# Kernel tuning notes

Hardware: AMD Instinct MI355X
Metric: run time of the kernel (lower is better)

## Reference

```python
import jax, jax.numpy as jnp
import numpy as np

N_NODES = 50000
N_EDGES = 500000
D_IN = 128
D_HID = 128
C = 1.0          # curvature (same for every layer)
MIN_NORM = 1e-15
MAX_TANH_ARG = 15.0
PROJ_EPS = 4e-3  # float32 boundary eps used by hgcn PoincareBall.proj


def _artanh(x):
    x = jnp.clip(x, -1.0 + 1e-7, 1.0 - 1e-7)
    return 0.5 * (jnp.log1p(x) - jnp.log1p(-x))


def _tanh(x):
    return jnp.tanh(jnp.clip(x, -MAX_TANH_ARG, MAX_TANH_ARG))


def _norm(x):
    return jnp.maximum(jnp.linalg.norm(x, axis=-1, keepdims=True), MIN_NORM)


def proj(x, c):
    # clip points to stay strictly inside the Poincare ball
    n = _norm(x)
    maxnorm = (1.0 - PROJ_EPS) / jnp.sqrt(c)
    return jnp.where(n > maxnorm, x / n * maxnorm, x)


def expmap0(u, c):
    sc = jnp.sqrt(c)
    n = _norm(u)
    return _tanh(sc * n) * u / (sc * n)


def logmap0(p, c):
    sc = jnp.sqrt(c)
    n = _norm(p)
    return _artanh(sc * n) * p / (sc * n)


def mobius_add(x, y, c):
    x2 = jnp.sum(x * x, -1, keepdims=True)
    y2 = jnp.sum(y * y, -1, keepdims=True)
    xy = jnp.sum(x * y, -1, keepdims=True)
    num = (1.0 + 2.0 * c * xy + c * y2) * x + (1.0 - c * x2) * y
    den = 1.0 + 2.0 * c * xy + c * c * x2 * y2
    return num / jnp.maximum(den, MIN_NORM)


def mobius_matvec(m, x, c):
    sc = jnp.sqrt(c)
    xn = _norm(x)
    mx = x @ m.T                                   # [N, out]
    mxn = _norm(mx)
    res = _tanh(mxn / xn * _artanh(sc * xn)) * mx / (mxn * sc)
    is_zero = jnp.all(mx == 0.0, axis=-1, keepdims=True)
    return jnp.where(is_zero, jnp.zeros_like(res), res)


def hyp_linear(x, W, b, c):
    h = proj(mobius_matvec(W, x, c), c)
    hyp_bias = proj(expmap0(b[None, :], c), c)     # proj_tan0 is identity on the ball
    return proj(mobius_add(h, hyp_bias, c), c)


def hyp_agg(x, src, dst, edge_weight, c):
    x_tan = logmap0(x, c)                          # [N, d] tangent at origin
    msg = edge_weight[:, None] * x_tan[src]        # [E, d] gather + scale
    agg = jax.ops.segment_sum(msg, dst, num_segments=N_NODES)  # spmm(adj, x_tan)
    return proj(expmap0(agg, c), c)


def hyp_act(x, c_in, c_out):
    xt = jax.nn.relu(logmap0(x, c_in))
    return proj(expmap0(xt, c_out), c_out)


def setup_inputs() -> dict:
    key = jax.random.key(0)
    ks = jax.random.split(key, 8)
    x = jax.random.normal(ks[0], (N_NODES, D_IN), dtype=jnp.float32) * 0.1
    src = jax.random.randint(ks[1], (N_EDGES,), 0, N_NODES)
    dst = jax.random.randint(ks[2], (N_EDGES,), 0, N_NODES)
    edge_weight = jax.random.uniform(ks[3], (N_EDGES,), dtype=jnp.float32) * 0.1
    s1 = 1.0 / np.sqrt(D_IN)
    W1 = jax.random.normal(ks[4], (D_HID, D_IN), dtype=jnp.float32) * s1
    b1 = jax.random.normal(ks[5], (D_HID,), dtype=jnp.float32) * 0.01
    W2 = jax.random.normal(ks[6], (D_HID, D_HID), dtype=jnp.float32) * s1
    b2 = jax.random.normal(ks[7], (D_HID,), dtype=jnp.float32) * 0.01
    return {"x": x, "src": src, "dst": dst, "edge_weight": edge_weight,
            "W1": W1, "b1": b1, "W2": W2, "b2": b2}


def reference(x, src, dst, edge_weight, W1, b1, W2, b2):
    c = jnp.float32(C)
    # HGCN.encode: proj_tan0 (identity for PoincareBall) -> expmap0 -> proj
    h = proj(expmap0(x, c), c)
    # layer 1: HypLinear -> HypAgg -> HypAct
    h = hyp_linear(h, W1, b1, c)
    h = hyp_agg(h, src, dst, edge_weight, c)
    h = hyp_act(h, c, c)
    # layer 2
    h = hyp_linear(h, W2, b2, c)
    h = hyp_agg(h, src, dst, edge_weight, c)
    h = hyp_act(h, c, c)
    return h
```

## Files before the change

kernel.cpp:

```cpp
#include <hip/hip_runtime.h>
#include <math.h>

#define MIN_NORM 1e-15f
#define MAXNORM  0.996f
#define ARTANH_CLIP 0.99999988f

typedef __bf16 bf16x8 __attribute__((ext_vector_type(8)));
typedef float  f32x4  __attribute__((ext_vector_type(4)));

union FragU { ushort u[8]; uint4 q; bf16x8 v; };

__device__ __forceinline__ float wave_sum(float v) {
#pragma unroll
    for (int off = 32; off > 0; off >>= 1) v += __shfl_xor(v, off, 64);
    return v;
}

__device__ __forceinline__ float artanh_c(float x) {
    x = fminf(fmaxf(x, -ARTANH_CLIP), ARTANH_CLIP);
    return 0.5f * (log1pf(x) - log1pf(-x));
}

__device__ __forceinline__ float tanh_c(float x) {
    return tanhf(fminf(fmaxf(x, -15.f), 15.f));
}

__device__ __forceinline__ float proj_factor(float n2) {
    float n = fmaxf(sqrtf(n2), MIN_NORM);
    return (n > MAXNORM) ? (MAXNORM / n) : 1.f;
}

__device__ __forceinline__ unsigned short f2bf(float f) {
    unsigned u = __float_as_uint(f);
    return (unsigned short)((u + 0x7fffu + ((u >> 16) & 1u)) >> 16);
}
__device__ __forceinline__ float bf2f(unsigned short h) {
    return __uint_as_float((unsigned)h << 16);
}

__device__ __forceinline__ void red16_f4(float4& v) {
#pragma unroll
    for (int off = 1; off < 16; off <<= 1) {
        v.x += __shfl_xor(v.x, off, 64);
        v.y += __shfl_xor(v.y, off, 64);
        v.z += __shfl_xor(v.z, off, 64);
        v.w += __shfl_xor(v.w, off, 64);
    }
}

__device__ __forceinline__ float bcast_row(const float4& v, int r) {
    const int src = (r >> 2) << 4;
    const float a = __shfl(v.x, src, 64);
    const float b = __shfl(v.y, src, 64);
    const float c = __shfl(v.z, src, 64);
    const float d = __shfl(v.w, src, 64);
    const float lo = (r & 1) ? b : a;
    const float hi = (r & 1) ? d : c;
    return (r & 2) ? hi : lo;
}

__device__ __forceinline__ void pack_w4(const float4 w4, int o, int k, char* out) {
    ushort4 h, l;
    h.x = f2bf(w4.x); l.x = f2bf(w4.x - bf2f(h.x));
    h.y = f2bf(w4.y); l.y = f2bf(w4.y - bf2f(h.y));
    h.z = f2bf(w4.z); l.z = f2bf(w4.z - bf2f(h.z));
    h.w = f2bf(w4.w); l.w = f2bf(w4.w - bf2f(h.w));
    const int prow = ((o & 7) << 4) | (o >> 3);
    const unsigned byte = (unsigned)((prow << 8) + (k << 1)) ^ (unsigned)((prow & 7) << 4);
    *reinterpret_cast<ushort4*>(out + byte) = h;
    *reinterpret_cast<ushort4*>(out + 32768 + byte) = l;
}

__global__ __launch_bounds__(256)
void setup_kernel(const float* __restrict__ W1, const float* __restrict__ W2,
                  char* __restrict__ g1, char* __restrict__ g2,
                  const float* __restrict__ b1, const float* __restrict__ b2,
                  float* __restrict__ hb1, float* __restrict__ hb2,
                  const int* __restrict__ dst, int* __restrict__ cnt, int E) {
    const int b = blockIdx.x;
    if (b < 32) {
        const float* W = (b < 16) ? W1 : W2;
        char* out = (b < 16) ? g1 : g2;
        const int i = (((b & 15) * 256) + threadIdx.x) * 4;
        pack_w4(*reinterpret_cast<const float4*>(&W[i]), i >> 7, i & 127, out);
    } else if (b == 32) {
        if (threadIdx.x < 64) {
            const int lane = threadIdx.x;
#pragma unroll
            for (int j = 0; j < 2; ++j) {
                const float* bb = j ? b2 : b1;
                float* hb = j ? hb2 : hb1;
                float v0 = bb[lane], v1 = bb[lane + 64];
                float n2 = wave_sum(v0 * v0 + v1 * v1);
                float n = fmaxf(sqrtf(n2), MIN_NORM);
                float sc = tanh_c(n) / n;
                sc *= proj_factor(sc * sc * n2);
                hb[lane] = v0 * sc;
                hb[lane + 64] = v1 * sc;
            }
        }
    } else {
        const int e = (b - 33) * 256 + threadIdx.x;
        if (e < E) atomicAdd(&cnt[dst[e]], 1);
    }
}


__global__ void scan1(const int* __restrict__ cnt, int* __restrict__ ptr,
                      int* __restrict__ bsum, int N) {
    __shared__ int s[256];
    const int t = threadIdx.x;
    const int i = blockIdx.x * 256 + t;
    int v = (i < N) ? cnt[i] : 0;
    s[t] = v;
    __syncthreads();
#pragma unroll
    for (int off = 1; off < 256; off <<= 1) {
        int add = (t >= off) ? s[t - off] : 0;
        __syncthreads();
        s[t] += add;
        __syncthreads();
    }
    if (i < N) ptr[i] = s[t] - v;
    if (t == 255) bsum[blockIdx.x] = s[255];
}

__global__ void scan2(const int* __restrict__ bsum, int* __restrict__ bscan, int nb) {
    __shared__ int s[256];
    const int t = threadIdx.x;
    int v = (t < nb) ? bsum[t] : 0;
    s[t] = v;
    __syncthreads();
#pragma unroll
    for (int off = 1; off < 256; off <<= 1) {
        int add = (t >= off) ? s[t - off] : 0;
        __syncthreads();
        s[t] += add;
        __syncthreads();
    }
    bscan[t] = s[t] - v;
}

__global__ void scan3(const int* __restrict__ bscan, int* __restrict__ ptr,
                      int* __restrict__ cursor, int N, int E) {
    const int i = blockIdx.x * blockDim.x + threadIdx.x;
    if (i < N) {
        const int p = ptr[i] + bscan[i >> 8];
        ptr[i] = p;
        cursor[i] = p;
    }
    if (i == 0) ptr[N] = E;
}

__global__ void scatter_kernel(const int* __restrict__ src, const int* __restrict__ dst,
                               const float* __restrict__ ew, int* __restrict__ cursor,
                               unsigned* __restrict__ epk, int E) {
    int e = blockIdx.x * blockDim.x + threadIdx.x;
    if (e >= E) return;
    int pos = atomicAdd(&cursor[dst[e]], 1);
    epk[pos] = ((unsigned)src[e] << 16) | (unsigned)f2bf(ew[e]);
}

template <bool PRELUDE, bool BF16OUT>
__global__ __launch_bounds__(1024, 4)
void hyp_linear_tan_mfma(const float* __restrict__ xin, const char* __restrict__ gWpack,
                         const float* __restrict__ hb, void* __restrict__ xtan,
                         int n_rows) {
    __shared__ __align__(16) char sW[65536];

    const int tid = threadIdx.x;
    const int lane = tid & 63, wid = tid >> 6;
    const int r15 = lane & 15, g = lane >> 4;

    const int tiles = (n_rows + 15) >> 4;
    const int tile = blockIdx.x + gridDim.x * wid;
    const bool active = (tile < tiles);
    const int rowbase = tile << 4;
    const int myrow = rowbase + r15;
    const bool rok = active && (myrow < n_rows);
    const float* xr = xin + (size_t)myrow * 128 + g * 8;

    float4 xa[4], xb[4];
#pragma unroll
    for (int kc = 0; kc < 4; ++kc) {
        if (rok) {
            xa[kc] = *reinterpret_cast<const float4*>(xr + kc * 32);
            xb[kc] = *reinterpret_cast<const float4*>(xr + kc * 32 + 4);
        } else {
            xa[kc] = make_float4(0.f, 0.f, 0.f, 0.f);
            xb[kc] = xa[kc];
        }
    }

    {
        const uint4* gsrc = reinterpret_cast<const uint4*>(gWpack);
        uint4* ldst = reinterpret_cast<uint4*>(sW);
#pragma unroll
        for (int i = 0; i < 4; ++i) ldst[tid + i * 1024] = gsrc[tid + i * 1024];
    }

    float yb[8];
    {
        const float4 yba = *reinterpret_cast<const float4*>(&hb[r15 * 8]);
        const float4 ybb = *reinterpret_cast<const float4*>(&hb[r15 * 8 + 4]);
        yb[0] = yba.x; yb[1] = yba.y; yb[2] = yba.z; yb[3] = yba.w;
        yb[4] = ybb.x; yb[5] = ybb.y; yb[6] = ybb.z; yb[7] = ybb.w;
    }
    float y2p = 0.f;
#pragma unroll
    for (int t = 0; t < 8; ++t) y2p += yb[t] * yb[t];
#pragma unroll
    for (int off = 1; off < 16; off <<= 1) y2p += __shfl_xor(y2p, off, 64);
    const float y2 = y2p;

    __syncthreads();
    if (!active) return;

    bf16x8 ah[4], al[4];
    float ss = 0.f;
#pragma unroll
    for (int kc = 0; kc < 4; ++kc) {
        const float4 a = xa[kc], b = xb[kc];
        ss += a.x * a.x + a.y * a.y + a.z * a.z + a.w * a.w
            + b.x * b.x + b.y * b.y + b.z * b.z + b.w * b.w;
        ah[kc][0] = (__bf16)a.x; al[kc][0] = (__bf16)(a.x - (float)ah[kc][0]);
        ah[kc][1] = (__bf16)a.y; al[kc][1] = (__bf16)(a.y - (float)ah[kc][1]);
        ah[kc][2] = (__bf16)a.z; al[kc][2] = (__bf16)(a.z - (float)ah[kc][2]);
        ah[kc][3] = (__bf16)a.w; al[kc][3] = (__bf16)(a.w - (float)ah[kc][3]);
        ah[kc][4] = (__bf16)b.x; al[kc][4] = (__bf16)(b.x - (float)ah[kc][4]);
        ah[kc][5] = (__bf16)b.y; al[kc][5] = (__bf16)(b.y - (float)ah[kc][5]);
        ah[kc][6] = (__bf16)b.z; al[kc][6] = (__bf16)(b.z - (float)ah[kc][6]);
        ah[kc][7] = (__bf16)b.w; al[kc][7] = (__bf16)(b.w - (float)ah[kc][7]);
    }
    ss += __shfl_xor(ss, 16, 64);
    ss += __shfl_xor(ss, 32, 64);

    f32x4 acc[8];
#pragma unroll
    for (int ct = 0; ct < 8; ++ct) acc[ct] = (f32x4){0.f, 0.f, 0.f, 0.f};

    const unsigned lswz = (unsigned)((r15 & 7) << 4);
#pragma unroll
    for (int kc = 0; kc < 4; ++kc) {
#pragma unroll
        for (int ct = 0; ct < 8; ++ct) {
            const unsigned byte =
                ((unsigned)((ct << 12) + (r15 << 8) + (kc << 6) + (g << 4))) ^ lswz;
            FragU bh, bl;
            bh.q = *reinterpret_cast<const uint4*>(sW + byte);
            bl.q = *reinterpret_cast<const uint4*>(sW + 32768 + byte);
            acc[ct] = __builtin_amdgcn_mfma_f32_16x16x32_bf16(ah[kc], bh.v, acc[ct], 0, 0, 0);
            acc[ct] = __builtin_amdgcn_mfma_f32_16x16x32_bf16(ah[kc], bl.v, acc[ct], 0, 0, 0);
            acc[ct] = __builtin_amdgcn_mfma_f32_16x16x32_bf16(al[kc], bh.v, acc[ct], 0, 0, 0);
        }
    }

    float4 r2 = make_float4(0.f, 0.f, 0.f, 0.f);
    float4 xyv = make_float4(0.f, 0.f, 0.f, 0.f);
#pragma unroll
    for (int ct = 0; ct < 8; ++ct) {
        r2.x += acc[ct][0] * acc[ct][0];
        r2.y += acc[ct][1] * acc[ct][1];
        r2.z += acc[ct][2] * acc[ct][2];
        r2.w += acc[ct][3] * acc[ct][3];
        xyv.x += acc[ct][0] * yb[ct];
        xyv.y += acc[ct][1] * yb[ct];
        xyv.z += acc[ct][2] * yb[ct];
        xyv.w += acc[ct][3] * yb[ct];
    }
    red16_f4(r2);
    red16_f4(xyv);

    const float rn2 = bcast_row(r2, r15);
    const float xyr = bcast_row(xyv, r15);
    const float n2v = ss;

    const float n = fmaxf(sqrtf(n2v), MIN_NORM);
    float sc = 1.f;
    if (PRELUDE) {
        sc = tanh_c(n) / n;
        sc *= proj_factor(sc * sc * n2v);
    }
    const float xn = fmaxf(sc * n, MIN_NORM);
    const float mxn = fmaxf(sc * sqrtf(rn2), MIN_NORM);
    const float s = tanh_c(mxn / xn * artanh_c(xn));
    const float sl0 = (s * sc) / mxn;
    float m2 = rn2 * sl0 * sl0;
    const float f = proj_factor(m2);
    const float scl = sl0 * f;
    m2 *= f * f;
    const float xy = scl * xyr;
    const float cx = 1.f + 2.f * xy + y2;
    const float cy = 1.f - m2;
    const float rdn = 1.f / fmaxf(1.f + 2.f * xy + m2 * y2, MIN_NORM);
    const float A = cx * scl * rdn;
    const float B = cy * rdn;
    const float on2 = A * A * rn2 + 2.f * A * B * xyr + B * B * y2;
    const float f2 = proj_factor(on2);
    const float onn = fmaxf(sqrtf(on2) * f2, MIN_NORM);
    const float slg = artanh_c(onn) / onn;
    const float P = slg * f2 * A;
    const float Q = slg * f2 * B;

#pragma unroll
    for (int reg = 0; reg < 4; ++reg) {
        const float Pr = __shfl(P, 4 * g + reg, 64);
        const float Qr = __shfl(Q, 4 * g + reg, 64);
        const int row = rowbase + 4 * g + reg;
        if (row < n_rows) {
            float v[8];
#pragma unroll
            for (int ct = 0; ct < 8; ++ct)
                v[ct] = fmaf(Pr, acc[ct][reg], Qr * yb[ct]);
            if (BF16OUT) {
                uint4 pk;
                pk.x = (unsigned)f2bf(v[0]) | ((unsigned)f2bf(v[1]) << 16);
                pk.y = (unsigned)f2bf(v[2]) | ((unsigned)f2bf(v[3]) << 16);
                pk.z = (unsigned)f2bf(v[4]) | ((unsigned)f2bf(v[5]) << 16);
                pk.w = (unsigned)f2bf(v[6]) | ((unsigned)f2bf(v[7]) << 16);
                *reinterpret_cast<uint4*>((char*)xtan + (size_t)row * 256 + r15 * 16) = pk;
            } else {
                float* orow = (float*)xtan + (size_t)row * 128 + r15 * 8;
                *reinterpret_cast<float4*>(orow) = make_float4(v[0], v[1], v[2], v[3]);
                *reinterpret_cast<float4*>(orow + 4) = make_float4(v[4], v[5], v[6], v[7]);
            }
        }
    }
}

__global__ __launch_bounds__(256)
void gather_act(const char* __restrict__ xt, const int* __restrict__ ptr,
                const unsigned* __restrict__ epk, float* __restrict__ out, int n_rows) {
    const int v = blockIdx.x * 4 + (threadIdx.x >> 6);
    if (v >= n_rows) return;
    const int lane = threadIdx.x & 63, l2 = lane << 1;
    const unsigned loff = (unsigned)lane << 2;
    const int beg = ptr[v], end = ptr[v + 1];
    float a0 = 0.f, a1 = 0.f, c0 = 0.f, c1 = 0.f;
    int i = beg;
    for (; i + 3 < end; i += 4) {
        const unsigned p0 = epk[i], p1 = epk[i + 1], p2 = epk[i + 2], p3 = epk[i + 3];
        const unsigned u0 = *reinterpret_cast<const unsigned*>(xt + ((p0 >> 16) << 8) + loff);
        const unsigned u1 = *reinterpret_cast<const unsigned*>(xt + ((p1 >> 16) << 8) + loff);
        const unsigned u2 = *reinterpret_cast<const unsigned*>(xt + ((p2 >> 16) << 8) + loff);
        const unsigned u3 = *reinterpret_cast<const unsigned*>(xt + ((p3 >> 16) << 8) + loff);
        const float w0 = __uint_as_float(p0 << 16), w1 = __uint_as_float(p1 << 16);
        const float w2 = __uint_as_float(p2 << 16), w3 = __uint_as_float(p3 << 16);
        a0 = fmaf(w0, __uint_as_float(u0 << 16), a0);
        a1 = fmaf(w0, __uint_as_float(u0 & 0xffff0000u), a1);
        c0 = fmaf(w1, __uint_as_float(u1 << 16), c0);
        c1 = fmaf(w1, __uint_as_float(u1 & 0xffff0000u), c1);
        a0 = fmaf(w2, __uint_as_float(u2 << 16), a0);
        a1 = fmaf(w2, __uint_as_float(u2 & 0xffff0000u), a1);
        c0 = fmaf(w3, __uint_as_float(u3 << 16), c0);
        c1 = fmaf(w3, __uint_as_float(u3 & 0xffff0000u), c1);
    }
    for (; i < end; ++i) {
        const unsigned p = epk[i];
        const unsigned u = *reinterpret_cast<const unsigned*>(xt + ((p >> 16) << 8) + loff);
        const float w = __uint_as_float(p << 16);
        a0 = fmaf(w, __uint_as_float(u << 16), a0);
        a1 = fmaf(w, __uint_as_float(u & 0xffff0000u), a1);
    }
    a0 += c0; a1 += c1;

    float n2 = wave_sum(a0 * a0 + a1 * a1);
    float n = fmaxf(sqrtf(n2), MIN_NORM);
    float sc = tanh_c(n) / n;
    float hn2 = sc * sc * n2;
    float f = proj_factor(hn2);
    sc *= f; hn2 *= f * f;
    float h0 = a0 * sc, h1 = a1 * sc;
    float hn = fmaxf(sqrtf(hn2), MIN_NORM);
    float sl = artanh_c(hn) / hn;
    float x0 = fmaxf(h0 * sl, 0.f), x1 = fmaxf(h1 * sl, 0.f);
    float n2b = wave_sum(x0 * x0 + x1 * x1);
    float nb = fmaxf(sqrtf(n2b), MIN_NORM);
    float scb = tanh_c(nb) / nb;
    scb *= proj_factor(scb * scb * n2b);
    *reinterpret_cast<float2*>(&out[(size_t)v * 128 + l2]) =
        make_float2(x0 * scb, x1 * scb);
}

__global__ __launch_bounds__(256)
void agg_edges(const float* __restrict__ xtan, const int* __restrict__ src,
               const int* __restrict__ dst, const float* __restrict__ ew,
               float* __restrict__ agg, int n_edges) {
    int gt = blockIdx.x * blockDim.x + threadIdx.x;
    int e = gt >> 5;
    if (e >= n_edges) return;
    int c = (gt & 31) << 2;
    int sN = src[e], dN = dst[e];
    float w = ew[e];
    const float4 v = *reinterpret_cast<const float4*>(&xtan[(size_t)sN * 128 + c]);
    float* ap = &agg[(size_t)dN * 128 + c];
    atomicAdd(ap + 0, w * v.x);
    atomicAdd(ap + 1, w * v.y);
    atomicAdd(ap + 2, w * v.z);
    atomicAdd(ap + 3, w * v.w);
}

__global__ __launch_bounds__(256)
void hyp_act_kernel(const float* __restrict__ in, float* __restrict__ out, int n_rows) {
    int row = blockIdx.x * 4 + (threadIdx.x >> 6);
    if (row >= n_rows) return;
    int lane = threadIdx.x & 63;
    int l2 = lane << 1;
    const float2 v = *reinterpret_cast<const float2*>(&in[(size_t)row * 128 + l2]);
    float a0 = v.x, a1 = v.y;
    float n2 = wave_sum(a0 * a0 + a1 * a1);
    float n = fmaxf(sqrtf(n2), MIN_NORM);
    float sc = tanh_c(n) / n;
    float hn2 = sc * sc * n2;
    float f = proj_factor(hn2);
    sc *= f; hn2 *= f * f;
    float h0 = a0 * sc, h1 = a1 * sc;
    float hn = fmaxf(sqrtf(hn2), MIN_NORM);
    float sl = artanh_c(hn) / hn;
    float x0 = fmaxf(h0 * sl, 0.f), x1 = fmaxf(h1 * sl, 0.f);
    float n2b = wave_sum(x0 * x0 + x1 * x1);
    float nb = fmaxf(sqrtf(n2b), MIN_NORM);
    float scb = tanh_c(nb) / nb;
    scb *= proj_factor(scb * scb * n2b);
    *reinterpret_cast<float2*>(&out[(size_t)row * 128 + l2]) =
        make_float2(x0 * scb, x1 * scb);
}

__global__ void bias_kernel(const float* __restrict__ b1, const float* __restrict__ b2,
                            float* __restrict__ hb1, float* __restrict__ hb2) {
    int lane = threadIdx.x;
#pragma unroll
    for (int j = 0; j < 2; ++j) {
        const float* b = j ? b2 : b1;
        float* hb = j ? hb2 : hb1;
        float v0 = b[lane], v1 = b[lane + 64];
        float n2 = wave_sum(v0 * v0 + v1 * v1);
        float n = fmaxf(sqrtf(n2), MIN_NORM);
        float sc = tanh_c(n) / n;
        sc *= proj_factor(sc * sc * n2);
        hb[lane] = v0 * sc;
        hb[lane + 64] = v1 * sc;
    }
}

__global__ void prep_w(const float* __restrict__ W1, const float* __restrict__ W2,
                       char* __restrict__ g1, char* __restrict__ g2) {
    const int b = blockIdx.x;
    const float* W = (b < 16) ? W1 : W2;
    char* out = (b < 16) ? g1 : g2;
    const int i = (((b & 15) * 256) + threadIdx.x) * 4;
    pack_w4(*reinterpret_cast<const float4*>(&W[i]), i >> 7, i & 127, out);
}

extern "C" void kernel_launch(void* const* d_in, const int* in_sizes, int n_in,
                              void* d_out, int out_size, void* d_ws, size_t ws_size,
                              hipStream_t stream) {
    const float* x   = (const float*)d_in[0];
    const int*   src = (const int*)d_in[1];
    const int*   dst = (const int*)d_in[2];
    const float* ew  = (const float*)d_in[3];
    const float* W1  = (const float*)d_in[4];
    const float* b1  = (const float*)d_in[5];
    const float* W2  = (const float*)d_in[6];
    const float* b2  = (const float*)d_in[7];

    const int N = in_sizes[0] / 128;
    const int E = in_sizes[1];
    float* fout = (float*)d_out;

    const int tiles = (N + 15) >> 4;
    int lin_grid = 256;
    while (lin_grid * 16 < tiles) lin_grid += 256;
    const int nbE = (E + 255) / 256;
    const int nbN = (N + 255) / 256;

    const size_t need = 131072 + 1024
                      + (size_t)N * 256 * 2
                      + (size_t)E * 4
                      + ((size_t)(N + 1) + N + N + 512) * 4;

    if (ws_size >= need) {
        char*  base  = (char*)d_ws;
        char*  gW1p  = base;
        char*  gW2p  = base + 65536;
        float* hb1   = (float*)(base + 131072);
        float* hb2   = hb1 + 128;
        char*  xtA   = base + 131072 + 1024;
        char*  xtB   = xtA + (size_t)N * 256;
        unsigned* epk = (unsigned*)(xtB + (size_t)N * 256);
        int* ptr     = (int*)(epk + E);
        int* cnt     = ptr + (N + 1);
        int* cursor  = cnt + N;
        int* bsum    = cursor + N;
        int* bscan   = bsum + 256;

        hipMemsetAsync(cnt, 0, (size_t)N * 4, stream);
        setup_kernel<<<33 + nbE, 256, 0, stream>>>(W1, W2, gW1p, gW2p,
                                                   b1, b2, hb1, hb2, dst, cnt, E);
        scan1<<<nbN, 256, 0, stream>>>(cnt, ptr, bsum, N);
        scan2<<<1, 256, 0, stream>>>(bsum, bscan, nbN);
        scan3<<<nbN, 256, 0, stream>>>(bscan, ptr, cursor, N, E);
        scatter_kernel<<<nbE, 256, 0, stream>>>(src, dst, ew, cursor, epk, E);

        hyp_linear_tan_mfma<true, true><<<lin_grid, 1024, 0, stream>>>(x, gW1p, hb1, xtA, N);
        gather_act<<<(N + 3) / 4, 256, 0, stream>>>(xtA, ptr, epk, fout, N);
        hyp_linear_tan_mfma<false, true><<<lin_grid, 1024, 0, stream>>>(fout, gW2p, hb2, xtB, N);
        gather_act<<<(N + 3) / 4, 256, 0, stream>>>(xtB, ptr, epk, fout, N);
    } else {
        char*  gW1p = (char*)d_ws;
        char*  gW2p = gW1p + 65536;
        float* hb1  = (float*)(gW2p + 65536);
        float* hb2  = hb1 + 128;
        float* nbuf = hb2 + 128;
        const size_t node_bytes = (size_t)N * 128 * sizeof(float);
        const int agg_blocks = (int)(((size_t)E * 32 + 255) / 256);
        const int row_blocks = (N + 3) / 4;

        prep_w<<<32, 256, 0, stream>>>(W1, W2, gW1p, gW2p);
        bias_kernel<<<1, 64, 0, stream>>>(b1, b2, hb1, hb2);
        hyp_linear_tan_mfma<true, false><<<lin_grid, 1024, 0, stream>>>(x, gW1p, hb1, fout, N);
        hipMemsetAsync(nbuf, 0, node_bytes, stream);
        agg_edges<<<agg_blocks, 256, 0, stream>>>(fout, src, dst, ew, nbuf, E);
        hyp_act_kernel<<<row_blocks, 256, 0, stream>>>(nbuf, nbuf, N);
        hyp_linear_tan_mfma<false, false><<<lin_grid, 1024, 0, stream>>>(nbuf, gW2p, hb2, fout, N);
        hipMemsetAsync(fout, 0, node_bytes, stream);
        agg_edges<<<agg_blocks, 256, 0, stream>>>(fout, src, dst, ew, nbuf, E);
        hyp_act_kernel<<<row_blocks, 256, 0, stream>>>(nbuf, fout, N);
    }
}
```

Measured before the change: 196.3 us.

## Pass bf16 activations between layers and restructure gather to 16-byte row loads

The intermediate activations between the first gather/activation and the second hyperbolic linear layer are now stored as bf16 instead of fp32. The second linear layer reads them directly as bf16 MFMA operands and drops the low-part correction MFMA. The gather kernel is reorganised so each wave handles four edges at once, with 16 lanes each loading a 16-byte slice of a row, prefetching the next packed edge and reducing across quarter-waves. This cuts memory traffic and MFMA work but adds bf16 rounding on the layer-1 output.

```diff
diff --git a/kernel.cpp b/kernel.cpp
--- a/kernel.cpp
+++ b/kernel.cpp
@@ -37,6 +37,8 @@
 __device__ __forceinline__ float bf2f(unsigned short h) {
     return __uint_as_float((unsigned)h << 16);
 }
+__device__ __forceinline__ float bflo(unsigned u) { return __uint_as_float(u << 16); }
+__device__ __forceinline__ float bfhi(unsigned u) { return __uint_as_float(u & 0xffff0000u); }
 
 __device__ __forceinline__ void red16_f4(float4& v) {
 #pragma unroll
@@ -161,9 +163,9 @@
     epk[pos] = ((unsigned)src[e] << 16) | (unsigned)f2bf(ew[e]);
 }
 
-template <bool PRELUDE, bool BF16OUT>
+template <bool PRELUDE, bool BF16IN, bool BF16OUT>
 __global__ __launch_bounds__(1024, 4)
-void hyp_linear_tan_mfma(const float* __restrict__ xin, const char* __restrict__ gWpack,
+void hyp_linear_tan_mfma(const void* __restrict__ xin, const char* __restrict__ gWpack,
                          const float* __restrict__ hb, void* __restrict__ xtan,
                          int n_rows) {
     __shared__ __align__(16) char sW[65536];
@@ -178,17 +180,26 @@
     const int rowbase = tile << 4;
     const int myrow = rowbase + r15;
     const bool rok = active && (myrow < n_rows);
-    const float* xr = xin + (size_t)myrow * 128 + g * 8;
 
     float4 xa[4], xb[4];
-#pragma unroll
-    for (int kc = 0; kc < 4; ++kc) {
-        if (rok) {
-            xa[kc] = *reinterpret_cast<const float4*>(xr + kc * 32);
-            xb[kc] = *reinterpret_cast<const float4*>(xr + kc * 32 + 4);
-        } else {
-            xa[kc] = make_float4(0.f, 0.f, 0.f, 0.f);
-            xb[kc] = xa[kc];
+    uint4 xu[4];
+    if (BF16IN) {
+        const char* xr = (const char*)xin + (size_t)myrow * 256 + g * 16;
+#pragma unroll
+        for (int kc = 0; kc < 4; ++kc)
+            xu[kc] = rok ? *reinterpret_cast<const uint4*>(xr + kc * 64)
+                         : make_uint4(0u, 0u, 0u, 0u);
+    } else {
+        const float* xr = (const float*)xin + (size_t)myrow * 128 + g * 8;
+#pragma unroll
+        for (int kc = 0; kc < 4; ++kc) {
+            if (rok) {
+                xa[kc] = *reinterpret_cast<const float4*>(xr + kc * 32);
+                xb[kc] = *reinterpret_cast<const float4*>(xr + kc * 32 + 4);
+            } else {
+                xa[kc] = make_float4(0.f, 0.f, 0.f, 0.f);
+                xb[kc] = xa[kc];
+            }
         }
     }
 
@@ -218,19 +229,32 @@
 
     bf16x8 ah[4], al[4];
     float ss = 0.f;
-#pragma unroll
-    for (int kc = 0; kc < 4; ++kc) {
-        const float4 a = xa[kc], b = xb[kc];
-        ss += a.x * a.x + a.y * a.y + a.z * a.z + a.w * a.w
-            + b.x * b.x + b.y * b.y + b.z * b.z + b.w * b.w;
-        ah[kc][0] = (__bf16)a.x; al[kc][0] = (__bf16)(a.x - (float)ah[kc][0]);
-        ah[kc][1] = (__bf16)a.y; al[kc][1] = (__bf16)(a.y - (float)ah[kc][1]);
-        ah[kc][2] = (__bf16)a.z; al[kc][2] = (__bf16)(a.z - (float)ah[kc][2]);
-        ah[kc][3] = (__bf16)a.w; al[kc][3] = (__bf16)(a.w - (float)ah[kc][3]);
-        ah[kc][4] = (__bf16)b.x; al[kc][4] = (__bf16)(b.x - (float)ah[kc][4]);
-        ah[kc][5] = (__bf16)b.y; al[kc][5] = (__bf16)(b.y - (float)ah[kc][5]);
-        ah[kc][6] = (__bf16)b.z; al[kc][6] = (__bf16)(b.z - (float)ah[kc][6]);
-        ah[kc][7] = (__bf16)b.w; al[kc][7] = (__bf16)(b.w - (float)ah[kc][7]);
+    if (BF16IN) {
+#pragma unroll
+        for (int kc = 0; kc < 4; ++kc) {
+            FragU fu; fu.q = xu[kc];
+            ah[kc] = fu.v;
+            const uint4 u = xu[kc];
+            float f0 = bflo(u.x), f1 = bfhi(u.x), f2_ = bflo(u.y), f3 = bfhi(u.y);
+            float f4 = bflo(u.z), f5 = bfhi(u.z), f6 = bflo(u.w), f7 = bfhi(u.w);
+            ss += f0 * f0 + f1 * f1 + f2_ * f2_ + f3 * f3
+                + f4 * f4 + f5 * f5 + f6 * f6 + f7 * f7;
+        }
+    } else {
+#pragma unroll
+        for (int kc = 0; kc < 4; ++kc) {
+            const float4 a = xa[kc], b = xb[kc];
+            ss += a.x * a.x + a.y * a.y + a.z * a.z + a.w * a.w
+                + b.x * b.x + b.y * b.y + b.z * b.z + b.w * b.w;
+            ah[kc][0] = (__bf16)a.x; al[kc][0] = (__bf16)(a.x - (float)ah[kc][0]);
+            ah[kc][1] = (__bf16)a.y; al[kc][1] = (__bf16)(a.y - (float)ah[kc][1]);
+            ah[kc][2] = (__bf16)a.z; al[kc][2] = (__bf16)(a.z - (float)ah[kc][2]);
+            ah[kc][3] = (__bf16)a.w; al[kc][3] = (__bf16)(a.w - (float)ah[kc][3]);
+            ah[kc][4] = (__bf16)b.x; al[kc][4] = (__bf16)(b.x - (float)ah[kc][4]);
+            ah[kc][5] = (__bf16)b.y; al[kc][5] = (__bf16)(b.y - (float)ah[kc][5]);
+            ah[kc][6] = (__bf16)b.z; al[kc][6] = (__bf16)(b.z - (float)ah[kc][6]);
+            ah[kc][7] = (__bf16)b.w; al[kc][7] = (__bf16)(b.w - (float)ah[kc][7]);
+        }
     }
     ss += __shfl_xor(ss, 16, 64);
     ss += __shfl_xor(ss, 32, 64);
@@ -251,7 +275,8 @@
             bl.q = *reinterpret_cast<const uint4*>(sW + 32768 + byte);
             acc[ct] = __builtin_amdgcn_mfma_f32_16x16x32_bf16(ah[kc], bh.v, acc[ct], 0, 0, 0);
             acc[ct] = __builtin_amdgcn_mfma_f32_16x16x32_bf16(ah[kc], bl.v, acc[ct], 0, 0, 0);
-            acc[ct] = __builtin_amdgcn_mfma_f32_16x16x32_bf16(al[kc], bh.v, acc[ct], 0, 0, 0);
+            if (!BF16IN)
+                acc[ct] = __builtin_amdgcn_mfma_f32_16x16x32_bf16(al[kc], bh.v, acc[ct], 0, 0, 0);
         }
     }
 
@@ -328,58 +353,82 @@
     }
 }
 
+template <bool BF16OUT>
 __global__ __launch_bounds__(256)
 void gather_act(const char* __restrict__ xt, const int* __restrict__ ptr,
-                const unsigned* __restrict__ epk, float* __restrict__ out, int n_rows) {
+                const unsigned* __restrict__ epk, void* __restrict__ out, int n_rows) {
     const int v = blockIdx.x * 4 + (threadIdx.x >> 6);
     if (v >= n_rows) return;
-    const int lane = threadIdx.x & 63, l2 = lane << 1;
-    const unsigned loff = (unsigned)lane << 2;
+    const int lane = threadIdx.x & 63;
+    const int q = lane >> 4, t = lane & 15;
+    const char* xtl = xt + (t << 4);
     const int beg = ptr[v], end = ptr[v + 1];
-    float a0 = 0.f, a1 = 0.f, c0 = 0.f, c1 = 0.f;
-    int i = beg;
-    for (; i + 3 < end; i += 4) {
-        const unsigned p0 = epk[i], p1 = epk[i + 1], p2 = epk[i + 2], p3 = epk[i + 3];
-        const unsigned u0 = *reinterpret_cast<const unsigned*>(xt + ((p0 >> 16) << 8) + loff);
-        const unsigned u1 = *reinterpret_cast<const unsigned*>(xt + ((p1 >> 16) << 8) + loff);
-        const unsigned u2 = *reinterpret_cast<const unsigned*>(xt + ((p2 >> 16) << 8) + loff);
-        const unsigned u3 = *reinterpret_cast<const unsigned*>(xt + ((p3 >> 16) << 8) + loff);
-        const float w0 = __uint_as_float(p0 << 16), w1 = __uint_as_float(p1 << 16);
-        const float w2 = __uint_as_float(p2 << 16), w3 = __uint_as_float(p3 << 16);
-        a0 = fmaf(w0, __uint_as_float(u0 << 16), a0);
-        a1 = fmaf(w0, __uint_as_float(u0 & 0xffff0000u), a1);
-        c0 = fmaf(w1, __uint_as_float(u1 << 16), c0);
-        c1 = fmaf(w1, __uint_as_float(u1 & 0xffff0000u), c1);
-        a0 = fmaf(w2, __uint_as_float(u2 << 16), a0);
-        a1 = fmaf(w2, __uint_as_float(u2 & 0xffff0000u), a1);
-        c0 = fmaf(w3, __uint_as_float(u3 << 16), c0);
-        c1 = fmaf(w3, __uint_as_float(u3 & 0xffff0000u), c1);
-    }
-    for (; i < end; ++i) {
-        const unsigned p = epk[i];
-        const unsigned u = *reinterpret_cast<const unsigned*>(xt + ((p >> 16) << 8) + loff);
+
+    float acc[8];
+#pragma unroll
+    for (int j = 0; j < 8; ++j) acc[j] = 0.f;
+
+    unsigned p = (beg + q < end) ? epk[beg + q] : 0u;
+    for (int i = beg; i < end; i += 4) {
+        const unsigned rowoff = (p & 0xffff0000u) >> 8;
+        const uint4 u = *reinterpret_cast<const uint4*>(xtl + rowoff);
+        const int en = i + 4 + q;
+        const unsigned pn = (en < end) ? epk[en] : 0u;
         const float w = __uint_as_float(p << 16);
-        a0 = fmaf(w, __uint_as_float(u << 16), a0);
-        a1 = fmaf(w, __uint_as_float(u & 0xffff0000u), a1);
-    }
-    a0 += c0; a1 += c1;
-
-    float n2 = wave_sum(a0 * a0 + a1 * a1);
+        acc[0] = fmaf(w, bflo(u.x), acc[0]);
+        acc[1] = fmaf(w, bfhi(u.x), acc[1]);
+        acc[2] = fmaf(w, bflo(u.y), acc[2]);
+        acc[3] = fmaf(w, bfhi(u.y), acc[3]);
+        acc[4] = fmaf(w, bflo(u.z), acc[4]);
+        acc[5] = fmaf(w, bfhi(u.z), acc[5]);
+        acc[6] = fmaf(w, bflo(u.w), acc[6]);
+        acc[7] = fmaf(w, bfhi(u.w), acc[7]);
+        p = pn;
+    }
+
+#pragma unroll
+    for (int j = 0; j < 8; ++j) {
+        acc[j] += __shfl_xor(acc[j], 16, 64);
+        acc[j] += __shfl_xor(acc[j], 32, 64);
+    }
+
+    float s = 0.f;
+#pragma unroll
+    for (int j = 0; j < 8; ++j) s += acc[j] * acc[j];
+#pragma unroll
+    for (int off = 1; off < 16; off <<= 1) s += __shfl_xor(s, off, 64);
+    const float n2 = s;
+
     float n = fmaxf(sqrtf(n2), MIN_NORM);
     float sc = tanh_c(n) / n;
     float hn2 = sc * sc * n2;
     float f = proj_factor(hn2);
     sc *= f; hn2 *= f * f;
-    float h0 = a0 * sc, h1 = a1 * sc;
     float hn = fmaxf(sqrtf(hn2), MIN_NORM);
     float sl = artanh_c(hn) / hn;
-    float x0 = fmaxf(h0 * sl, 0.f), x1 = fmaxf(h1 * sl, 0.f);
-    float n2b = wave_sum(x0 * x0 + x1 * x1);
-    float nb = fmaxf(sqrtf(n2b), MIN_NORM);
+    const float scl1 = sc * sl;
+
+    float x[8];
+    float s2 = 0.f;
+#pragma unroll
+    for (int j = 0; j < 8; ++j) {
+        x[j] = fmaxf(acc[j] * scl1, 0.f);
+        s2 += x[j] * x[j];
+    }
+#pragma unroll
+    for (int off = 1; off < 16; off <<= 1) s2 += __shfl_xor(s2, off, 64);
+    float nb = fmaxf(sqrtf(s2), MIN_NORM);
     float scb = tanh_c(nb) / nb;
-    scb *= proj_factor(scb * scb * n2b);
-    *reinterpret_cast<float2*>(&out[(size_t)v * 128 + l2]) =
-        make_float2(x0 * scb, x1 * scb);
+    scb *= proj_factor(scb * scb * s2);
+
+    const float o0 = x[2 * q] * scb, o1 = x[2 * q + 1] * scb;
+    if (BF16OUT) {
+        const unsigned pk = (unsigned)f2bf(o0) | ((unsigned)f2bf(o1) << 16);
+        *reinterpret_cast<unsigned*>((char*)out + (size_t)v * 256 + t * 16 + q * 4) = pk;
+    } else {
+        *reinterpret_cast<float2*>((float*)out + (size_t)v * 128 + t * 8 + q * 2) =
+            make_float2(o0, o1);
+    }
 }
 
 __global__ __launch_bounds__(256)
@@ -502,10 +551,10 @@
         scan3<<<nbN, 256, 0, stream>>>(bscan, ptr, cursor, N, E);
         scatter_kernel<<<nbE, 256, 0, stream>>>(src, dst, ew, cursor, epk, E);
 
-        hyp_linear_tan_mfma<true, true><<<lin_grid, 1024, 0, stream>>>(x, gW1p, hb1, xtA, N);
-        gather_act<<<(N + 3) / 4, 256, 0, stream>>>(xtA, ptr, epk, fout, N);
-        hyp_linear_tan_mfma<false, true><<<lin_grid, 1024, 0, stream>>>(fout, gW2p, hb2, xtB, N);
-        gather_act<<<(N + 3) / 4, 256, 0, stream>>>(xtB, ptr, epk, fout, N);
+        hyp_linear_tan_mfma<true, false, true><<<lin_grid, 1024, 0, stream>>>(x, gW1p, hb1, xtA, N);
+        gather_act<true><<<(N + 3) / 4, 256, 0, stream>>>(xtA, ptr, epk, xtB, N);
+        hyp_linear_tan_mfma<false, true, true><<<lin_grid, 1024, 0, stream>>>(xtB, gW2p, hb2, xtA, N);
+        gather_act<false><<<(N + 3) / 4, 256, 0, stream>>>(xtA, ptr, epk, fout, N);
     } else {
         char*  gW1p = (char*)d_ws;
         char*  gW2p = gW1p + 65536;
@@ -518,11 +567,11 @@
 
         prep_w<<<32, 256, 0, stream>>>(W1, W2, gW1p, gW2p);
         bias_kernel<<<1, 64, 0, stream>>>(b1, b2, hb1, hb2);
-        hyp_linear_tan_mfma<true, false><<<lin_grid, 1024, 0, stream>>>(x, gW1p, hb1, fout, N);
+        hyp_linear_tan_mfma<true, false, false><<<lin_grid, 1024, 0, stream>>>(x, gW1p, hb1, fout, N);
         hipMemsetAsync(nbuf, 0, node_bytes, stream);
         agg_edges<<<agg_blocks, 256, 0, stream>>>(fout, src, dst, ew, nbuf, E);
         hyp_act_kernel<<<row_blocks, 256, 0, stream>>>(nbuf, nbuf, N);
-        hyp_linear_tan_mfma<false, false><<<lin_grid, 1024, 0, stream>>>(nbuf, gW2p, hb2, fout, N);
+        hyp_linear_tan_mfma<false, false, false><<<lin_grid, 1024, 0, stream>>>(nbuf, gW2p, hb2, fout, N);
         hipMemsetAsync(fout, 0, node_bytes, stream);
         agg_edges<<<agg_blocks, 256, 0, stream>>>(fout, src, dst, ew, nbuf, E);
         hyp_act_kernel<<<row_blocks, 256, 0, stream>>>(nbuf, fout, N);
```

New measurement: 194.9 us. About the same (-0.7%).
